# Kernel optimization log

Measured on AMD Instinct MI355X. Metric: run time of the kernel, lower is better.

## Reference

```python
import jax, jax.numpy as jnp
import numpy as np

V, E, H, O, B, T = 50000, 128, 128, 128, 64, 512


def setup_inputs() -> dict:
    key = jax.random.key(0)
    ks = jax.random.split(key, 16)
    s = 0.05
    X = jax.random.randint(ks[0], (B, T), 0, V)
    lens = jnp.sort(jax.random.randint(ks[1], (B,), 64, T + 1))[::-1]
    lens = lens.at[0].set(T)  # pack_padded needs descending lengths, max == T
    emb = jax.random.normal(ks[2], (V, E)) * s
    emb = emb.at[0].set(0.0)  # padding_idx = 0
    return {
        "X": X,
        "X_lengths": lens,
        "batch_size": B,
        "emb": emb,
        "W_e2i": jax.random.normal(ks[3], (H, E)) * s,
        "b_e2i": jax.random.normal(ks[4], (H,)) * s,
        "Wih_f": jax.random.normal(ks[5], (3 * H, H)) * s,
        "Whh_f": jax.random.normal(ks[6], (3 * H, H)) * s,
        "bih_f": jax.random.normal(ks[7], (3 * H,)) * s,
        "bhh_f": jax.random.normal(ks[8], (3 * H,)) * s,
        "Wih_b": jax.random.normal(ks[9], (3 * H, H)) * s,
        "Whh_b": jax.random.normal(ks[10], (3 * H, H)) * s,
        "bih_b": jax.random.normal(ks[11], (3 * H,)) * s,
        "bhh_b": jax.random.normal(ks[12], (3 * H,)) * s,
        "W_h2o": jax.random.normal(ks[13], (O, 2 * H)) * s,
        "b_h2o": jax.random.normal(ks[14], (O,)) * s,
        "u_w": jax.random.uniform(ks[15], (O,)),  # torch.rand
    }


def _gru_scan(gx, mask_tb, Whh, bhh):
    """gx: [T,B,3H] precomputed input gates; mask_tb: [T,B,1] valid-step mask.
    Masked update emulates pack_padded_sequence: padded steps keep h unchanged
    (and h stays 0 before the first valid step of the reversed direction)."""
    h0 = jnp.zeros((gx.shape[1], Whh.shape[1]), gx.dtype)

    def step(h, tb):
        gxt, m = tb
        gh = h @ Whh.T + bhh
        gxr, gxz, gxn = jnp.split(gxt, 3, axis=-1)
        ghr, ghz, ghn = jnp.split(gh, 3, axis=-1)
        r = jax.nn.sigmoid(gxr + ghr)
        z = jax.nn.sigmoid(gxz + ghz)
        n = jnp.tanh(gxn + r * ghn)
        h_new = (1.0 - z) * n + z * h
        h = jnp.where(m, h_new, h)
        return h, h

    _, hs = jax.lax.scan(step, h0, (gx, mask_tb))
    return hs  # [T,B,H]


def reference(X, X_lengths, batch_size, emb, W_e2i, b_e2i,
              Wih_f, Whh_f, bih_f, bhh_f, Wih_b, Whh_b, bih_b, bhh_b,
              W_h2o, b_h2o, u_w):
    x = emb[X]                              # [B,T,E]
    x = x @ W_e2i.T + b_e2i                 # [B,T,H]
    Tn = x.shape[1]
    mask = jnp.arange(Tn)[None, :] < X_lengths[:, None]  # [B,T]
    m_tb = mask.T[:, :, None]               # [T,B,1]

    gx_f = (x @ Wih_f.T + bih_f).transpose(1, 0, 2)       # [T,B,3H]
    h_f = _gru_scan(gx_f, m_tb, Whh_f, bhh_f)             # [T,B,H]
    gx_b = (x @ Wih_b.T + bih_b).transpose(1, 0, 2)[::-1]
    h_b = _gru_scan(gx_b, m_tb[::-1], Whh_b, bhh_b)[::-1]

    Hout = jnp.concatenate([h_f, h_b], axis=-1).transpose(1, 0, 2)  # [B,T,2H]
    Hout = Hout * mask[:, :, None].astype(Hout.dtype)  # pad_packed zeros pads

    Y = jnp.tanh(Hout @ W_h2o.T + b_h2o)               # [B,T,O]
    scores = jnp.where(mask, (Y * u_w).sum(-1), -jnp.inf)  # [B,T]
    alpha = jax.nn.softmax(scores, axis=1)             # per-sample softmax over valid steps
    pooled = jnp.einsum("bt,btd->bd", alpha, Hout)     # [B,2H]
    return pooled[None]                                # [1,B,2H]
```

## Files before the change

### kernel.cpp

```cpp
#include <hip/hip_runtime.h>
#include <hip/hip_bf16.h>

#define VV 50000
#define EE 128
#define HH 128
#define OO 128
#define BB 64
#define TT 512

typedef __bf16 bf16_t;
typedef __attribute__((ext_vector_type(8))) __bf16 bf16x8;
typedef __attribute__((ext_vector_type(4))) __bf16 bf16x4;
typedef __attribute__((ext_vector_type(4))) float floatx4;

#define SC_RZ (-1.4426950408889634f)
#define SC_N  (2.8853900817779268f)

__device__ __forceinline__ bf16x8 ldb8(const bf16_t* p) {
    return *reinterpret_cast<const bf16x8*>(p);
}

__device__ __forceinline__ bf16x8 ldf8_bf(const float* p) {
    const float4* q = reinterpret_cast<const float4*>(p);
    float4 u = q[0], v = q[1];
    bf16x8 r;
    r[0] = (__bf16)u.x; r[1] = (__bf16)u.y; r[2] = (__bf16)u.z; r[3] = (__bf16)u.w;
    r[4] = (__bf16)v.x; r[5] = (__bf16)v.y; r[6] = (__bf16)v.z; r[7] = (__bf16)v.w;
    return r;
}

__device__ __forceinline__ float fast_rcp(float x) { return __builtin_amdgcn_rcpf(x); }
__device__ __forceinline__ float exp2_f(float x) { return __builtin_amdgcn_exp2f(x); }
__device__ __forceinline__ float tanh_f(float x) {
    float e = __expf(2.0f * x);
    return 1.0f - 2.0f * fast_rcp(e + 1.0f);
}

__device__ __forceinline__ void lds_barrier() {
    asm volatile("s_waitcnt lgkmcnt(0)\n\ts_barrier" ::: "memory");
}

__global__ __launch_bounds__(256) void k0_conv(
    const float* __restrict__ we,
    const float* __restrict__ wihf, const float* __restrict__ wihb,
    const float* __restrict__ whhf, const float* __restrict__ whhb,
    const float* __restrict__ wh2o,
    const float* __restrict__ bihf, const float* __restrict__ bhhf,
    const float* __restrict__ bihb, const float* __restrict__ bhhb,
    bf16_t* __restrict__ we_bf,
    bf16_t* __restrict__ wih_bf, bf16_t* __restrict__ whh_bf,
    bf16_t* __restrict__ wh2o_bf, float* __restrict__ gxbias) {
    int tid = blockIdx.x * 256 + threadIdx.x;
    int np = gridDim.x * 256;
    for (int i = tid; i < HH * EE; i += np) we_bf[i] = (bf16_t)we[i];
    for (int i = tid; i < 384 * HH; i += np) {
        int nrow = i >> 7;
        float sc = (nrow < 256) ? SC_RZ : SC_N;
        wih_bf[i] = (bf16_t)(sc * wihf[i]);
        wih_bf[384 * HH + i] = (bf16_t)(sc * wihb[i]);
        whh_bf[i] = (bf16_t)(sc * whhf[i]);
        whh_bf[384 * HH + i] = (bf16_t)(sc * whhb[i]);
    }
    for (int i = tid; i < OO * 256; i += np) wh2o_bf[i] = (bf16_t)wh2o[i];
    if (tid < 768) {
        int dir = tid / 384, n = tid % 384;
        const float* bih = dir ? bihb : bihf;
        const float* bhh = dir ? bhhb : bhhf;
        float sc = (n < 256) ? SC_RZ : SC_N;
        gxbias[tid] = sc * bih[n] + (n < 256 ? sc * bhh[n] : 0.0f);
    }
}

__global__ __launch_bounds__(256) void k12_gx(const int* __restrict__ X,
                                              const float* __restrict__ emb,
                                              const bf16_t* __restrict__ we_bf,
                                              const float* __restrict__ be,
                                              const bf16_t* __restrict__ wih_bf,
                                              const float* __restrict__ gxbias,
                                              const int* __restrict__ lens,
                                              bf16_t* __restrict__ gx3) {
    int blk = blockIdx.x;
    int tq = blk >> 2;
    int g = blk & 3;
    if (4 * tq >= lens[16 * g]) return;

    int lane = threadIdx.x & 63;
    int w2 = threadIdx.x >> 6;
    int quad = lane >> 4, col = lane & 15;

    __shared__ bf16_t xs[4][16 * 136];

#pragma unroll
    for (int tt = 0; tt < 4; ++tt) {
        int t = 4 * tq + tt;
        int v = X[(g * 16 + col) * TT + t];
        bf16x8 a[4];
#pragma unroll
        for (int kc = 0; kc < 4; ++kc)
            a[kc] = ldf8_bf(emb + (size_t)v * EE + kc * 32 + quad * 8);
#pragma unroll
        for (int tl = 0; tl < 2; ++tl) {
            int n = 32 * w2 + 16 * tl + col;
            floatx4 acc = {0.f, 0.f, 0.f, 0.f};
#pragma unroll
            for (int kc = 0; kc < 4; ++kc) {
                bf16x8 bw = ldb8(we_bf + (size_t)n * EE + kc * 32 + quad * 8);
                acc = __builtin_amdgcn_mfma_f32_16x16x32_bf16(a[kc], bw, acc, 0, 0, 0);
            }
            float bias = be[n];
#pragma unroll
            for (int r = 0; r < 4; ++r)
                xs[tt][(quad * 4 + r) * 136 + n] = (bf16_t)(acc[r] + bias);
        }
    }
    __syncthreads();

    bf16x8 a2[4][4];
#pragma unroll
    for (int tt = 0; tt < 4; ++tt)
#pragma unroll
        for (int kc = 0; kc < 4; ++kc)
            a2[tt][kc] = ldb8(xs[tt] + col * 136 + kc * 32 + quad * 8);

#pragma unroll 2
    for (int tl = 0; tl < 12; ++tl) {
        int idx = w2 * 12 + tl;
        int dir = idx >= 24;
        int n = (idx - dir * 24) * 16 + col;
        bf16x8 bw[4];
#pragma unroll
        for (int kc = 0; kc < 4; ++kc)
            bw[kc] = ldb8(wih_bf + ((size_t)dir * 384 + n) * HH + kc * 32 + quad * 8);
        float bias = gxbias[dir * 384 + n];
#pragma unroll
        for (int tt = 0; tt < 4; ++tt) {
            int t = 4 * tq + tt;
            floatx4 acc = {0.f, 0.f, 0.f, 0.f};
#pragma unroll
            for (int kc = 0; kc < 4; ++kc)
                acc = __builtin_amdgcn_mfma_f32_16x16x32_bf16(a2[tt][kc], bw[kc], acc, 0, 0, 0);
            bf16x4 pack;
#pragma unroll
            for (int r = 0; r < 4; ++r)
                pack[r] = (__bf16)(acc[r] + bias);
            *reinterpret_cast<bf16x4*>(
                gx3 + (((size_t)(dir * 16 + 4 * g + quad) * TT + t) * 384 + n) * 4) = pack;
        }
    }
}

#define HPAD 144
#define HBUF (4 * HPAD)
__global__ __launch_bounds__(512) void k3_gru(const bf16_t* __restrict__ gx3,
                                              const bf16_t* __restrict__ whh_bf,
                                              const float* __restrict__ bhh_f,
                                              const float* __restrict__ bhh_b,
                                              const int* __restrict__ lens,
                                              bf16_t* __restrict__ hist2) {
    int g16 = blockIdx.x;
    int dir = blockIdx.y;
    const float* bhh = dir ? bhh_b : bhh_f;

    int tid = threadIdx.x;
    int w = tid >> 6;
    int lane = tid & 63;
    int quad = lane >> 4, col = lane & 15;
    int j = 16 * w + col;

    __shared__ bf16_t hl[2 * HBUF];
    for (int i = tid; i < 2 * HBUF; i += 512) hl[i] = (bf16_t)0.f;

    int len1 = lens[4 * g16 + quad];
    int Lmax = max(max(lens[4 * g16], lens[4 * g16 + 1]),
                   max(lens[4 * g16 + 2], lens[4 * g16 + 3]));

    float bhn = SC_N * bhh[256 + j];

    bf16x8 Bw[3][4];
#pragma unroll
    for (int gate = 0; gate < 3; ++gate)
#pragma unroll
        for (int kc = 0; kc < 4; ++kc)
            Bw[gate][kc] = ldb8(whh_bf + ((size_t)dir * 384 + gate * 128 + j) * HH + kc * 32 + quad * 8);

    const bf16_t* gbase = gx3 + (size_t)(dir * 16 + g16) * TT * 1536;
    bf16_t* hb = hist2 + (size_t)(dir * 16 + g16) * TT * 512;
    int loff[3];
#pragma unroll
    for (int gate = 0; gate < 3; ++gate)
        loff[gate] = (gate * 128 + j) * 4 + quad;
    int hoff = quad * 128 + j;
    int aoff = (col >> 2) * HPAD + quad * 8;

    float h = 0.f;
    int S4 = (Lmax + 3) & ~3;

    __bf16 ring[4][3];
#pragma unroll
    for (int u = 0; u < 4; ++u) {
        int t = dir ? (Lmax - 1 - u) : u;
#pragma unroll
        for (int gate = 0; gate < 3; ++gate)
            ring[u][gate] = gbase[(size_t)t * 1536 + loff[gate]];
    }
    lds_barrier();

    int gstep = dir ? -1536 : 1536;
    int hstep = dir ? -512 : 512;
    const bf16_t* rp0 = gbase + (size_t)(dir ? (Lmax - 5) : 4) * 1536 + loff[0];
    const bf16_t* rp1 = gbase + (size_t)(dir ? (Lmax - 5) : 4) * 1536 + loff[1];
    const bf16_t* rp2 = gbase + (size_t)(dir ? (Lmax - 5) : 4) * 1536 + loff[2];
    bf16_t* hp = hb + (size_t)(dir ? (Lmax - 1) : 0) * 512 + hoff;
    int ulo = dir ? (Lmax - len1) : 0;
    int uhi = dir ? Lmax : len1;

    for (int sb = 0; sb < S4; sb += 4) {
#pragma unroll
        for (int u = 0; u < 4; ++u) {
            int s = sb + u;
            const bf16_t* hc = hl + (s & 1) * HBUF;
            bf16_t* hn = hl + ((s + 1) & 1) * HBUF;

            float gx0 = (float)ring[u][0];
            float gx1 = (float)ring[u][1];
            float gx2 = (float)ring[u][2];

            bf16x8 a[4];
#pragma unroll
            for (int kc = 0; kc < 4; ++kc)
                a[kc] = ldb8(hc + aoff + kc * 32);

            floatx4 cr = {0.f, 0.f, 0.f, 0.f};
            floatx4 cz = {0.f, 0.f, 0.f, 0.f};
            floatx4 cn = {bhn, bhn, bhn, bhn};
#pragma unroll
            for (int kc = 0; kc < 4; ++kc) {
                cr = __builtin_amdgcn_mfma_f32_16x16x32_bf16(a[kc], Bw[0][kc], cr, 0, 0, 0);
                cz = __builtin_amdgcn_mfma_f32_16x16x32_bf16(a[kc], Bw[1][kc], cz, 0, 0, 0);
                cn = __builtin_amdgcn_mfma_f32_16x16x32_bf16(a[kc], Bw[2][kc], cn, 0, 0, 0);
            }

            ring[u][0] = *rp0;
            ring[u][1] = *rp1;
            ring[u][2] = *rp2;
            {
                int adv = (s < Lmax - 5) ? gstep : 0;
                rp0 += adv; rp1 += adv; rp2 += adv;
            }

            float rg = fast_rcp(1.0f + exp2_f(cr[0] + gx0));
            float zg = fast_rcp(1.0f + exp2_f(cz[0] + gx1));
            float v  = fmaf(rg, cn[0], gx2);
            float ng = fmaf(-2.0f, fast_rcp(exp2_f(v) + 1.0f), 1.0f);
            float hnew = fmaf(zg, h - ng, ng);

            bool upd = (s >= ulo) && (s < uhi);
            h = upd ? hnew : h;
            bf16_t h16 = (bf16_t)h;
            hn[quad * HPAD + j] = h16;
            *hp = h16;
            hp += (s < Lmax - 1) ? hstep : 0;

            lds_barrier();
        }
    }
}

__global__ __launch_bounds__(512) void k45_pool(const bf16_t* __restrict__ hist2,
                                                const bf16_t* __restrict__ wh2o_bf,
                                                const float* __restrict__ bh2o,
                                                const float* __restrict__ uw,
                                                const int* __restrict__ lens,
                                                float* __restrict__ out) {
    int b = blockIdx.x;
    int g16 = b >> 2, bl = b & 3;
    int tid = threadIdx.x;
    int lane = tid & 63, w3 = tid >> 6;
    int quad = lane >> 4, col = lane & 15;
    int len = lens[b];

    int p = w3 >> 2;
    int q = w3 & 3;

    __shared__ float smax[TT][4];
    __shared__ float alpha[TT];
    __shared__ float red[512];
    __shared__ float red2[16 * 32 * 8];

    const bf16_t* hf = hist2 + (size_t)g16 * TT * 512 + bl * 128;
    const bf16_t* hbk = hist2 + (size_t)(16 + g16) * TT * 512 + bl * 128;

    int n0 = (q * 2 + 0) * 16 + col;
    int n1 = (q * 2 + 1) * 16 + col;
    float bias0 = bh2o[n0], u0 = uw[n0];
    float bias1 = bh2o[n1], u1 = uw[n1];

    bf16x8 bw0[8], bw1[8];
#pragma unroll
    for (int kc = 0; kc < 8; ++kc) {
        bw0[kc] = ldb8(wh2o_bf + (size_t)n0 * 256 + kc * 32 + quad * 8);
        bw1[kc] = ldb8(wh2o_bf + (size_t)n1 * 256 + kc * 32 + quad * 8);
    }

    int nch = (len + 15) >> 4;
    bf16x8 a[8], an[8];
    {
        int t = p * 16 + col;
#pragma unroll
        for (int kc = 0; kc < 4; ++kc) {
            a[kc]     = ldb8(hf  + (size_t)t * 512 + kc * 32 + quad * 8);
            a[kc + 4] = ldb8(hbk + (size_t)t * 512 + kc * 32 + quad * 8);
        }
    }
    for (int ch = p; ch < nch; ch += 2) {
        int t0 = ch * 16;
        {
            int tn = (ch + 2 < nch ? t0 + 32 : t0) + col;
#pragma unroll
            for (int kc = 0; kc < 4; ++kc) {
                an[kc]     = ldb8(hf  + (size_t)tn * 512 + kc * 32 + quad * 8);
                an[kc + 4] = ldb8(hbk + (size_t)tn * 512 + kc * 32 + quad * 8);
            }
        }
        float p4[4] = {0.f, 0.f, 0.f, 0.f};
#pragma unroll
        for (int tl = 0; tl < 2; ++tl) {
            float bias = tl ? bias1 : bias0;
            float u = tl ? u1 : u0;
            floatx4 acc = {0.f, 0.f, 0.f, 0.f};
#pragma unroll
            for (int kc = 0; kc < 8; ++kc) {
                bf16x8 bw = tl ? bw1[kc] : bw0[kc];
                acc = __builtin_amdgcn_mfma_f32_16x16x32_bf16(a[kc], bw, acc, 0, 0, 0);
            }
#pragma unroll
            for (int r = 0; r < 4; ++r)
                p4[r] += tanh_f(acc[r] + bias) * u;
        }
#pragma unroll
        for (int m = 1; m < 16; m <<= 1)
#pragma unroll
            for (int r = 0; r < 4; ++r)
                p4[r] += __shfl_xor(p4[r], m, 64);
        if (col == 0) {
#pragma unroll
            for (int r = 0; r < 4; ++r)
                smax[t0 + quad * 4 + r][q] = p4[r];
        }
#pragma unroll
        for (int kc = 0; kc < 8; ++kc) a[kc] = an[kc];
    }
    __syncthreads();

    int t = tid;
    float s = -1e30f;
    if (t < len) s = smax[t][0] + smax[t][1] + smax[t][2] + smax[t][3];
    red[tid] = s;
    __syncthreads();
    for (int st = 256; st > 0; st >>= 1) {
        if (tid < st) red[tid] = fmaxf(red[tid], red[tid + st]);
        __syncthreads();
    }
    float mx = red[0];
    __syncthreads();
    float e = (t < len) ? __expf(s - mx) : 0.f;
    alpha[t] = e;
    red[tid] = e;
    __syncthreads();
    for (int st = 256; st > 0; st >>= 1) {
        if (tid < st) red[tid] += red[tid + st];
        __syncthreads();
    }
    float inv = fast_rcp(red[0]);
    __syncthreads();

    {
        int ts = tid >> 5, o = tid & 31;
        int dirp = o >> 4;
        int j8 = (o & 15) * 8;
        const bf16_t* hbase = (dirp ? hbk : hf) + j8;
        float acc8[8];
#pragma unroll
        for (int ee = 0; ee < 8; ++ee) acc8[ee] = 0.f;
        for (int tt2 = ts; tt2 < len; tt2 += 16) {
            float al = alpha[tt2];
            bf16x8 hv = ldb8(hbase + (size_t)tt2 * 512);
#pragma unroll
            for (int ee = 0; ee < 8; ++ee) acc8[ee] = fmaf(al, (float)hv[ee], acc8[ee]);
        }
#pragma unroll
        for (int ee = 0; ee < 8; ++ee) red2[(ts * 32 + o) * 8 + ee] = acc8[ee];
        __syncthreads();
        if (tid < 256) {
            int c = tid;
            int dir2 = c >> 7, rem = c & 127;
            int oo = dir2 * 16 + (rem >> 3), ee = c & 7;
            float acc = 0.f;
#pragma unroll
            for (int qq = 0; qq < 16; ++qq) acc += red2[(qq * 32 + oo) * 8 + ee];
            out[(size_t)b * 256 + c] = acc * inv;
        }
    }
}

extern "C" void kernel_launch(void* const* d_in, const int* in_sizes, int n_in,
                              void* d_out, int out_size, void* d_ws, size_t ws_size,
                              hipStream_t stream) {
    const int* X       = (const int*)d_in[0];
    const int* lens    = (const int*)d_in[1];
    const float* emb   = (const float*)d_in[3];
    const float* We2i  = (const float*)d_in[4];
    const float* be2i  = (const float*)d_in[5];
    const float* Wihf  = (const float*)d_in[6];
    const float* Whhf  = (const float*)d_in[7];
    const float* bihf  = (const float*)d_in[8];
    const float* bhhf  = (const float*)d_in[9];
    const float* Wihb  = (const float*)d_in[10];
    const float* Whhb  = (const float*)d_in[11];
    const float* bihb  = (const float*)d_in[12];
    const float* bhhb  = (const float*)d_in[13];
    const float* Wh2o  = (const float*)d_in[14];
    const float* bh2o  = (const float*)d_in[15];
    const float* uw    = (const float*)d_in[16];

    char* ws = (char*)d_ws;
    size_t off = 0;
    bf16_t* we_bf = (bf16_t*)(ws + off);   off += (size_t)HH * EE * 2;
    bf16_t* wih_bf = (bf16_t*)(ws + off);  off += (size_t)2 * 384 * HH * 2;
    bf16_t* whh_bf = (bf16_t*)(ws + off);  off += (size_t)2 * 384 * HH * 2;
    bf16_t* wh2o_bf = (bf16_t*)(ws + off); off += (size_t)OO * 256 * 2;
    float* gxbias = (float*)(ws + off);    off += 768 * 4;
    off = (off + 255) & ~(size_t)255;
    bf16_t* gx3 = (bf16_t*)(ws + off);     off += (size_t)32 * TT * 384 * 4 * 2;
    bf16_t* hist2 = (bf16_t*)(ws + off);   off += (size_t)32 * TT * 4 * 128 * 2;

    float* out = (float*)d_out;

    k0_conv<<<dim3(256), dim3(256), 0, stream>>>(We2i, Wihf, Wihb, Whhf, Whhb,
                                                 Wh2o, bihf, bhhf, bihb, bhhb,
                                                 we_bf, wih_bf, whh_bf, wh2o_bf, gxbias);
    k12_gx<<<dim3(TT), dim3(256), 0, stream>>>(X, emb, we_bf, be2i, wih_bf, gxbias, lens, gx3);
    k3_gru<<<dim3(16, 2), dim3(512), 0, stream>>>(gx3, whh_bf, bhhf, bhhb, lens, hist2);
    k45_pool<<<dim3(BB), dim3(512), 0, stream>>>(hist2, wh2o_bf, bh2o, uw, lens, out);
}
```

Measured before the change: 342.1 us.

## Drop weight-conversion kernel and convert fp32 weights to bf16 inside consumers

Removes the separate k0_conv launch that pre-converted and pre-scaled all weights to bf16. Each consumer kernel now loads the fp32 weights and applies the scale and bf16 conversion itself, and the gate biases are folded on the fly. k12_gx also goes from 256 to 512 threads, so each wave handles fewer output tiles. This saves one kernel launch plus its global write/read round trip, but it doubles weight-load bytes and adds conversion work inside the other kernels.

```diff
diff --git a/kernel.cpp b/kernel.cpp
--- a/kernel.cpp
+++ b/kernel.cpp
@@ -29,6 +29,17 @@
     return r;
 }
 
+__device__ __forceinline__ bf16x8 ldf8s(const float* p, float s) {
+    const float4* q = reinterpret_cast<const float4*>(p);
+    float4 u = q[0], v = q[1];
+    bf16x8 r;
+    r[0] = (__bf16)(s * u.x); r[1] = (__bf16)(s * u.y);
+    r[2] = (__bf16)(s * u.z); r[3] = (__bf16)(s * u.w);
+    r[4] = (__bf16)(s * v.x); r[5] = (__bf16)(s * v.y);
+    r[6] = (__bf16)(s * v.z); r[7] = (__bf16)(s * v.w);
+    return r;
+}
+
 __device__ __forceinline__ float fast_rcp(float x) { return __builtin_amdgcn_rcpf(x); }
 __device__ __forceinline__ float exp2_f(float x) { return __builtin_amdgcn_exp2f(x); }
 __device__ __forceinline__ float tanh_f(float x) {
@@ -40,43 +51,16 @@
     asm volatile("s_waitcnt lgkmcnt(0)\n\ts_barrier" ::: "memory");
 }
 
-__global__ __launch_bounds__(256) void k0_conv(
-    const float* __restrict__ we,
-    const float* __restrict__ wihf, const float* __restrict__ wihb,
-    const float* __restrict__ whhf, const float* __restrict__ whhb,
-    const float* __restrict__ wh2o,
-    const float* __restrict__ bihf, const float* __restrict__ bhhf,
-    const float* __restrict__ bihb, const float* __restrict__ bhhb,
-    bf16_t* __restrict__ we_bf,
-    bf16_t* __restrict__ wih_bf, bf16_t* __restrict__ whh_bf,
-    bf16_t* __restrict__ wh2o_bf, float* __restrict__ gxbias) {
-    int tid = blockIdx.x * 256 + threadIdx.x;
-    int np = gridDim.x * 256;
-    for (int i = tid; i < HH * EE; i += np) we_bf[i] = (bf16_t)we[i];
-    for (int i = tid; i < 384 * HH; i += np) {
-        int nrow = i >> 7;
-        float sc = (nrow < 256) ? SC_RZ : SC_N;
-        wih_bf[i] = (bf16_t)(sc * wihf[i]);
-        wih_bf[384 * HH + i] = (bf16_t)(sc * wihb[i]);
-        whh_bf[i] = (bf16_t)(sc * whhf[i]);
-        whh_bf[384 * HH + i] = (bf16_t)(sc * whhb[i]);
-    }
-    for (int i = tid; i < OO * 256; i += np) wh2o_bf[i] = (bf16_t)wh2o[i];
-    if (tid < 768) {
-        int dir = tid / 384, n = tid % 384;
-        const float* bih = dir ? bihb : bihf;
-        const float* bhh = dir ? bhhb : bhhf;
-        float sc = (n < 256) ? SC_RZ : SC_N;
-        gxbias[tid] = sc * bih[n] + (n < 256 ? sc * bhh[n] : 0.0f);
-    }
-}
-
-__global__ __launch_bounds__(256) void k12_gx(const int* __restrict__ X,
+__global__ __launch_bounds__(512) void k12_gx(const int* __restrict__ X,
                                               const float* __restrict__ emb,
-                                              const bf16_t* __restrict__ we_bf,
+                                              const float* __restrict__ we,
                                               const float* __restrict__ be,
-                                              const bf16_t* __restrict__ wih_bf,
-                                              const float* __restrict__ gxbias,
+                                              const float* __restrict__ wihf,
+                                              const float* __restrict__ wihb,
+                                              const float* __restrict__ bihf,
+                                              const float* __restrict__ bhhf,
+                                              const float* __restrict__ bihb,
+                                              const float* __restrict__ bhhb,
                                               const int* __restrict__ lens,
                                               bf16_t* __restrict__ gx3) {
     int blk = blockIdx.x;
@@ -84,30 +68,30 @@
     int g = blk & 3;
     if (4 * tq >= lens[16 * g]) return;
 
-    int lane = threadIdx.x & 63;
-    int w2 = threadIdx.x >> 6;
+    int tid = threadIdx.x;
+    int lane = tid & 63;
+    int w = tid >> 6;
     int quad = lane >> 4, col = lane & 15;
 
     __shared__ bf16_t xs[4][16 * 136];
 
-#pragma unroll
-    for (int tt = 0; tt < 4; ++tt) {
-        int t = 4 * tq + tt;
-        int v = X[(g * 16 + col) * TT + t];
-        bf16x8 a[4];
-#pragma unroll
-        for (int kc = 0; kc < 4; ++kc)
-            a[kc] = ldf8_bf(emb + (size_t)v * EE + kc * 32 + quad * 8);
-#pragma unroll
-        for (int tl = 0; tl < 2; ++tl) {
-            int n = 32 * w2 + 16 * tl + col;
+    {
+        int n = 16 * w + col;
+        float bias = be[n];
+#pragma unroll
+        for (int tt = 0; tt < 4; ++tt) {
+            int t = 4 * tq + tt;
+            int v = X[(g * 16 + col) * TT + t];
+            bf16x8 a[4];
+#pragma unroll
+            for (int kc = 0; kc < 4; ++kc)
+                a[kc] = ldf8_bf(emb + (size_t)v * EE + kc * 32 + quad * 8);
             floatx4 acc = {0.f, 0.f, 0.f, 0.f};
 #pragma unroll
             for (int kc = 0; kc < 4; ++kc) {
-                bf16x8 bw = ldb8(we_bf + (size_t)n * EE + kc * 32 + quad * 8);
+                bf16x8 bw = ldf8_bf(we + (size_t)n * EE + kc * 32 + quad * 8);
                 acc = __builtin_amdgcn_mfma_f32_16x16x32_bf16(a[kc], bw, acc, 0, 0, 0);
             }
-            float bias = be[n];
 #pragma unroll
             for (int r = 0; r < 4; ++r)
                 xs[tt][(quad * 4 + r) * 136 + n] = (bf16_t)(acc[r] + bias);
@@ -123,15 +107,19 @@
             a2[tt][kc] = ldb8(xs[tt] + col * 136 + kc * 32 + quad * 8);
 
 #pragma unroll 2
-    for (int tl = 0; tl < 12; ++tl) {
-        int idx = w2 * 12 + tl;
+    for (int tl = 0; tl < 6; ++tl) {
+        int idx = w * 6 + tl;
         int dir = idx >= 24;
         int n = (idx - dir * 24) * 16 + col;
+        const float* wih = dir ? wihb : wihf;
+        const float* bih = dir ? bihb : bihf;
+        const float* bhh = dir ? bhhb : bhhf;
+        float sc = (n < 256) ? SC_RZ : SC_N;
         bf16x8 bw[4];
 #pragma unroll
         for (int kc = 0; kc < 4; ++kc)
-            bw[kc] = ldb8(wih_bf + ((size_t)dir * 384 + n) * HH + kc * 32 + quad * 8);
-        float bias = gxbias[dir * 384 + n];
+            bw[kc] = ldf8s(wih + (size_t)n * HH + kc * 32 + quad * 8, sc);
+        float bias = sc * (bih[n] + (n < 256 ? bhh[n] : 0.0f));
 #pragma unroll
         for (int tt = 0; tt < 4; ++tt) {
             int t = 4 * tq + tt;
@@ -152,7 +140,8 @@
 #define HPAD 144
 #define HBUF (4 * HPAD)
 __global__ __launch_bounds__(512) void k3_gru(const bf16_t* __restrict__ gx3,
-                                              const bf16_t* __restrict__ whh_bf,
+                                              const float* __restrict__ whh_f,
+                                              const float* __restrict__ whh_b,
                                               const float* __restrict__ bhh_f,
                                               const float* __restrict__ bhh_b,
                                               const int* __restrict__ lens,
@@ -160,6 +149,7 @@
     int g16 = blockIdx.x;
     int dir = blockIdx.y;
     const float* bhh = dir ? bhh_b : bhh_f;
+    const float* whh = dir ? whh_b : whh_f;
 
     int tid = threadIdx.x;
     int w = tid >> 6;
@@ -178,10 +168,12 @@
 
     bf16x8 Bw[3][4];
 #pragma unroll
-    for (int gate = 0; gate < 3; ++gate)
+    for (int gate = 0; gate < 3; ++gate) {
+        float sc = (gate < 2) ? SC_RZ : SC_N;
 #pragma unroll
         for (int kc = 0; kc < 4; ++kc)
-            Bw[gate][kc] = ldb8(whh_bf + ((size_t)dir * 384 + gate * 128 + j) * HH + kc * 32 + quad * 8);
+            Bw[gate][kc] = ldf8s(whh + (size_t)(gate * 128 + j) * HH + kc * 32 + quad * 8, sc);
+    }
 
     const bf16_t* gbase = gx3 + (size_t)(dir * 16 + g16) * TT * 1536;
     bf16_t* hb = hist2 + (size_t)(dir * 16 + g16) * TT * 512;
@@ -267,7 +259,7 @@
 }
 
 __global__ __launch_bounds__(512) void k45_pool(const bf16_t* __restrict__ hist2,
-                                                const bf16_t* __restrict__ wh2o_bf,
+                                                const float* __restrict__ wh2o,
                                                 const float* __restrict__ bh2o,
                                                 const float* __restrict__ uw,
                                                 const int* __restrict__ lens,
@@ -298,8 +290,8 @@
     bf16x8 bw0[8], bw1[8];
 #pragma unroll
     for (int kc = 0; kc < 8; ++kc) {
-        bw0[kc] = ldb8(wh2o_bf + (size_t)n0 * 256 + kc * 32 + quad * 8);
-        bw1[kc] = ldb8(wh2o_bf + (size_t)n1 * 256 + kc * 32 + quad * 8);
+        bw0[kc] = ldf8_bf(wh2o + (size_t)n0 * 256 + kc * 32 + quad * 8);
+        bw1[kc] = ldf8_bf(wh2o + (size_t)n1 * 256 + kc * 32 + quad * 8);
     }
 
     int nch = (len + 15) >> 4;
@@ -425,21 +417,13 @@
 
     char* ws = (char*)d_ws;
     size_t off = 0;
-    bf16_t* we_bf = (bf16_t*)(ws + off);   off += (size_t)HH * EE * 2;
-    bf16_t* wih_bf = (bf16_t*)(ws + off);  off += (size_t)2 * 384 * HH * 2;
-    bf16_t* whh_bf = (bf16_t*)(ws + off);  off += (size_t)2 * 384 * HH * 2;
-    bf16_t* wh2o_bf = (bf16_t*)(ws + off); off += (size_t)OO * 256 * 2;
-    float* gxbias = (float*)(ws + off);    off += 768 * 4;
-    off = (off + 255) & ~(size_t)255;
     bf16_t* gx3 = (bf16_t*)(ws + off);     off += (size_t)32 * TT * 384 * 4 * 2;
     bf16_t* hist2 = (bf16_t*)(ws + off);   off += (size_t)32 * TT * 4 * 128 * 2;
 
     float* out = (float*)d_out;
 
-    k0_conv<<<dim3(256), dim3(256), 0, stream>>>(We2i, Wihf, Wihb, Whhf, Whhb,
-                                                 Wh2o, bihf, bhhf, bihb, bhhb,
-                                                 we_bf, wih_bf, whh_bf, wh2o_bf, gxbias);
-    k12_gx<<<dim3(TT), dim3(256), 0, stream>>>(X, emb, we_bf, be2i, wih_bf, gxbias, lens, gx3);
-    k3_gru<<<dim3(16, 2), dim3(512), 0, stream>>>(gx3, whh_bf, bhhf, bhhb, lens, hist2);
-    k45_pool<<<dim3(BB), dim3(512), 0, stream>>>(hist2, wh2o_bf, bh2o, uw, lens, out);
-}
+    k12_gx<<<dim3(TT), dim3(512), 0, stream>>>(X, emb, We2i, be2i, Wihf, Wihb,
+                                               bihf, bhhf, bihb, bhhb, lens, gx3);
+    k3_gru<<<dim3(16, 2), dim3(512), 0, stream>>>(gx3, Whhf, Whhb, bhhf, bhhb, lens, hist2);
+    k45_pool<<<dim3(BB), dim3(512), 0, stream>>>(hist2, Wh2o, bh2o, uw, lens, out);
+}
```

Result: slower. 387.9 us (+13.4%).

## Fuse GRU recurrence and attention pooling into one kernel with atomic grid barrier

Applied to the files above, without the earlier changes.

Merges the GRU scan kernel and the attention-pooling kernel into a single 64-block launch. The first 32 blocks run the recurrence, then every block spin-waits on a global atomic counter, which is reset in the gx kernel, before doing its per-sample pooling. This removes one launch and its gap, but the wait relies on all 64 blocks being co-resident. It also redistributes the embedding projection across waves in k12, splits the h2o MFMA chain into two accumulators, replaces the shared-memory tree reductions with wave shuffles, and pads red2 to avoid bank conflicts.

```diff
diff --git a/kernel.cpp b/kernel.cpp
--- a/kernel.cpp
+++ b/kernel.cpp
@@ -78,7 +78,10 @@
                                               const bf16_t* __restrict__ wih_bf,
                                               const float* __restrict__ gxbias,
                                               const int* __restrict__ lens,
-                                              bf16_t* __restrict__ gx3) {
+                                              bf16_t* __restrict__ gx3,
+                                              unsigned int* __restrict__ ctr) {
+    if (blockIdx.x == 0 && threadIdx.x == 0) *ctr = 0u;
+
     int blk = blockIdx.x;
     int tq = blk >> 2;
     int g = blk & 3;
@@ -90,17 +93,16 @@
 
     __shared__ bf16_t xs[4][16 * 136];
 
-#pragma unroll
-    for (int tt = 0; tt < 4; ++tt) {
-        int t = 4 * tq + tt;
+    {
+        int t = 4 * tq + w2;
         int v = X[(g * 16 + col) * TT + t];
         bf16x8 a[4];
 #pragma unroll
         for (int kc = 0; kc < 4; ++kc)
             a[kc] = ldf8_bf(emb + (size_t)v * EE + kc * 32 + quad * 8);
 #pragma unroll
-        for (int tl = 0; tl < 2; ++tl) {
-            int n = 32 * w2 + 16 * tl + col;
+        for (int nt = 0; nt < 8; ++nt) {
+            int n = nt * 16 + col;
             floatx4 acc = {0.f, 0.f, 0.f, 0.f};
 #pragma unroll
             for (int kc = 0; kc < 4; ++kc) {
@@ -110,7 +112,7 @@
             float bias = be[n];
 #pragma unroll
             for (int r = 0; r < 4; ++r)
-                xs[tt][(quad * 4 + r) * 136 + n] = (bf16_t)(acc[r] + bias);
+                xs[w2][(quad * 4 + r) * 136 + n] = (bf16_t)(acc[r] + bias);
         }
     }
     __syncthreads();
@@ -151,254 +153,265 @@
 
 #define HPAD 144
 #define HBUF (4 * HPAD)
-__global__ __launch_bounds__(512) void k3_gru(const bf16_t* __restrict__ gx3,
-                                              const bf16_t* __restrict__ whh_bf,
-                                              const float* __restrict__ bhh_f,
-                                              const float* __restrict__ bhh_b,
-                                              const int* __restrict__ lens,
-                                              bf16_t* __restrict__ hist2) {
-    int g16 = blockIdx.x;
-    int dir = blockIdx.y;
-    const float* bhh = dir ? bhh_b : bhh_f;
-
+__global__ __launch_bounds__(512) void k345(const bf16_t* __restrict__ gx3,
+                                            const bf16_t* __restrict__ whh_bf,
+                                            const float* __restrict__ bhh_f,
+                                            const float* __restrict__ bhh_b,
+                                            const int* __restrict__ lens,
+                                            const bf16_t* __restrict__ wh2o_bf,
+                                            const float* __restrict__ bh2o,
+                                            const float* __restrict__ uw,
+                                            bf16_t* __restrict__ hist2,
+                                            float* __restrict__ out,
+                                            unsigned int* __restrict__ ctr) {
+    int b = blockIdx.x;
     int tid = threadIdx.x;
-    int w = tid >> 6;
     int lane = tid & 63;
+    int wv = tid >> 6;
     int quad = lane >> 4, col = lane & 15;
-    int j = 16 * w + col;
 
     __shared__ bf16_t hl[2 * HBUF];
-    for (int i = tid; i < 2 * HBUF; i += 512) hl[i] = (bf16_t)0.f;
-
-    int len1 = lens[4 * g16 + quad];
-    int Lmax = max(max(lens[4 * g16], lens[4 * g16 + 1]),
-                   max(lens[4 * g16 + 2], lens[4 * g16 + 3]));
-
-    float bhn = SC_N * bhh[256 + j];
-
-    bf16x8 Bw[3][4];
-#pragma unroll
-    for (int gate = 0; gate < 3; ++gate)
-#pragma unroll
-        for (int kc = 0; kc < 4; ++kc)
-            Bw[gate][kc] = ldb8(whh_bf + ((size_t)dir * 384 + gate * 128 + j) * HH + kc * 32 + quad * 8);
-
-    const bf16_t* gbase = gx3 + (size_t)(dir * 16 + g16) * TT * 1536;
-    bf16_t* hb = hist2 + (size_t)(dir * 16 + g16) * TT * 512;
-    int loff[3];
-#pragma unroll
-    for (int gate = 0; gate < 3; ++gate)
-        loff[gate] = (gate * 128 + j) * 4 + quad;
-    int hoff = quad * 128 + j;
-    int aoff = (col >> 2) * HPAD + quad * 8;
-
-    float h = 0.f;
-    int S4 = (Lmax + 3) & ~3;
-
-    __bf16 ring[4][3];
-#pragma unroll
-    for (int u = 0; u < 4; ++u) {
-        int t = dir ? (Lmax - 1 - u) : u;
-#pragma unroll
-        for (int gate = 0; gate < 3; ++gate)
-            ring[u][gate] = gbase[(size_t)t * 1536 + loff[gate]];
-    }
-    lds_barrier();
-
-    int gstep = dir ? -1536 : 1536;
-    int hstep = dir ? -512 : 512;
-    const bf16_t* rp0 = gbase + (size_t)(dir ? (Lmax - 5) : 4) * 1536 + loff[0];
-    const bf16_t* rp1 = gbase + (size_t)(dir ? (Lmax - 5) : 4) * 1536 + loff[1];
-    const bf16_t* rp2 = gbase + (size_t)(dir ? (Lmax - 5) : 4) * 1536 + loff[2];
-    bf16_t* hp = hb + (size_t)(dir ? (Lmax - 1) : 0) * 512 + hoff;
-    int ulo = dir ? (Lmax - len1) : 0;
-    int uhi = dir ? Lmax : len1;
-
-    for (int sb = 0; sb < S4; sb += 4) {
-#pragma unroll
-        for (int u = 0; u < 4; ++u) {
-            int s = sb + u;
-            const bf16_t* hc = hl + (s & 1) * HBUF;
-            bf16_t* hn = hl + ((s + 1) & 1) * HBUF;
-
-            float gx0 = (float)ring[u][0];
-            float gx1 = (float)ring[u][1];
-            float gx2 = (float)ring[u][2];
-
-            bf16x8 a[4];
-#pragma unroll
-            for (int kc = 0; kc < 4; ++kc)
-                a[kc] = ldb8(hc + aoff + kc * 32);
-
-            floatx4 cr = {0.f, 0.f, 0.f, 0.f};
-            floatx4 cz = {0.f, 0.f, 0.f, 0.f};
-            floatx4 cn = {bhn, bhn, bhn, bhn};
-#pragma unroll
-            for (int kc = 0; kc < 4; ++kc) {
-                cr = __builtin_amdgcn_mfma_f32_16x16x32_bf16(a[kc], Bw[0][kc], cr, 0, 0, 0);
-                cz = __builtin_amdgcn_mfma_f32_16x16x32_bf16(a[kc], Bw[1][kc], cz, 0, 0, 0);
-                cn = __builtin_amdgcn_mfma_f32_16x16x32_bf16(a[kc], Bw[2][kc], cn, 0, 0, 0);
-            }
-
-            ring[u][0] = *rp0;
-            ring[u][1] = *rp1;
-            ring[u][2] = *rp2;
-            {
-                int adv = (s < Lmax - 5) ? gstep : 0;
-                rp0 += adv; rp1 += adv; rp2 += adv;
-            }
-
-            float rg = fast_rcp(1.0f + exp2_f(cr[0] + gx0));
-            float zg = fast_rcp(1.0f + exp2_f(cz[0] + gx1));
-            float v  = fmaf(rg, cn[0], gx2);
-            float ng = fmaf(-2.0f, fast_rcp(exp2_f(v) + 1.0f), 1.0f);
-            float hnew = fmaf(zg, h - ng, ng);
-
-            bool upd = (s >= ulo) && (s < uhi);
-            h = upd ? hnew : h;
-            bf16_t h16 = (bf16_t)h;
-            hn[quad * HPAD + j] = h16;
-            *hp = h16;
-            hp += (s < Lmax - 1) ? hstep : 0;
-
-            lds_barrier();
-        }
-    }
-}
-
-__global__ __launch_bounds__(512) void k45_pool(const bf16_t* __restrict__ hist2,
-                                                const bf16_t* __restrict__ wh2o_bf,
-                                                const float* __restrict__ bh2o,
-                                                const float* __restrict__ uw,
-                                                const int* __restrict__ lens,
-                                                float* __restrict__ out) {
-    int b = blockIdx.x;
-    int g16 = b >> 2, bl = b & 3;
-    int tid = threadIdx.x;
-    int lane = tid & 63, w3 = tid >> 6;
-    int quad = lane >> 4, col = lane & 15;
-    int len = lens[b];
-
-    int p = w3 >> 2;
-    int q = w3 & 3;
-
     __shared__ float smax[TT][4];
     __shared__ float alpha[TT];
-    __shared__ float red[512];
-    __shared__ float red2[16 * 32 * 8];
-
-    const bf16_t* hf = hist2 + (size_t)g16 * TT * 512 + bl * 128;
-    const bf16_t* hbk = hist2 + (size_t)(16 + g16) * TT * 512 + bl * 128;
-
-    int n0 = (q * 2 + 0) * 16 + col;
-    int n1 = (q * 2 + 1) * 16 + col;
-    float bias0 = bh2o[n0], u0 = uw[n0];
-    float bias1 = bh2o[n1], u1 = uw[n1];
-
-    bf16x8 bw0[8], bw1[8];
-#pragma unroll
-    for (int kc = 0; kc < 8; ++kc) {
-        bw0[kc] = ldb8(wh2o_bf + (size_t)n0 * 256 + kc * 32 + quad * 8);
-        bw1[kc] = ldb8(wh2o_bf + (size_t)n1 * 256 + kc * 32 + quad * 8);
-    }
-
-    int nch = (len + 15) >> 4;
-    bf16x8 a[8], an[8];
+    __shared__ float redw[16];
+    __shared__ float red2[16 * 32 * 9];
+
+    if (b < 32) {
+        int g16 = b & 15;
+        int dir = b >> 4;
+        const float* bhh = dir ? bhh_b : bhh_f;
+        int j = 16 * wv + col;
+
+        for (int i = tid; i < 2 * HBUF; i += 512) hl[i] = (bf16_t)0.f;
+
+        int len1 = lens[4 * g16 + quad];
+        int Lmax = max(max(lens[4 * g16], lens[4 * g16 + 1]),
+                       max(lens[4 * g16 + 2], lens[4 * g16 + 3]));
+
+        float bhn = SC_N * bhh[256 + j];
+
+        bf16x8 Bw[3][4];
+#pragma unroll
+        for (int gate = 0; gate < 3; ++gate)
+#pragma unroll
+            for (int kc = 0; kc < 4; ++kc)
+                Bw[gate][kc] = ldb8(whh_bf + ((size_t)dir * 384 + gate * 128 + j) * HH + kc * 32 + quad * 8);
+
+        const bf16_t* gbase = gx3 + (size_t)(dir * 16 + g16) * TT * 1536;
+        bf16_t* hb = hist2 + (size_t)(dir * 16 + g16) * TT * 512;
+        int loff[3];
+#pragma unroll
+        for (int gate = 0; gate < 3; ++gate)
+            loff[gate] = (gate * 128 + j) * 4 + quad;
+        int hoff = quad * 128 + j;
+        int aoff = (col >> 2) * HPAD + quad * 8;
+
+        float h = 0.f;
+        int S4 = (Lmax + 3) & ~3;
+
+        __bf16 ring[4][3];
+#pragma unroll
+        for (int u = 0; u < 4; ++u) {
+            int t = dir ? (Lmax - 1 - u) : u;
+#pragma unroll
+            for (int gate = 0; gate < 3; ++gate)
+                ring[u][gate] = gbase[(size_t)t * 1536 + loff[gate]];
+        }
+        lds_barrier();
+
+        int gstep = dir ? -1536 : 1536;
+        int hstep = dir ? -512 : 512;
+        const bf16_t* rp0 = gbase + (size_t)(dir ? (Lmax - 5) : 4) * 1536 + loff[0];
+        const bf16_t* rp1 = gbase + (size_t)(dir ? (Lmax - 5) : 4) * 1536 + loff[1];
+        const bf16_t* rp2 = gbase + (size_t)(dir ? (Lmax - 5) : 4) * 1536 + loff[2];
+        bf16_t* hp = hb + (size_t)(dir ? (Lmax - 1) : 0) * 512 + hoff;
+        int ulo = dir ? (Lmax - len1) : 0;
+        int uhi = dir ? Lmax : len1;
+
+        for (int sb = 0; sb < S4; sb += 4) {
+#pragma unroll
+            for (int u = 0; u < 4; ++u) {
+                int s = sb + u;
+                const bf16_t* hc = hl + (s & 1) * HBUF;
+                bf16_t* hn = hl + ((s + 1) & 1) * HBUF;
+
+                float gx0 = (float)ring[u][0];
+                float gx1 = (float)ring[u][1];
+                float gx2 = (float)ring[u][2];
+
+                bf16x8 a[4];
+#pragma unroll
+                for (int kc = 0; kc < 4; ++kc)
+                    a[kc] = ldb8(hc + aoff + kc * 32);
+
+                floatx4 cr = {0.f, 0.f, 0.f, 0.f};
+                floatx4 cz = {0.f, 0.f, 0.f, 0.f};
+                floatx4 cn = {bhn, bhn, bhn, bhn};
+#pragma unroll
+                for (int kc = 0; kc < 4; ++kc) {
+                    cr = __builtin_amdgcn_mfma_f32_16x16x32_bf16(a[kc], Bw[0][kc], cr, 0, 0, 0);
+                    cz = __builtin_amdgcn_mfma_f32_16x16x32_bf16(a[kc], Bw[1][kc], cz, 0, 0, 0);
+                    cn = __builtin_amdgcn_mfma_f32_16x16x32_bf16(a[kc], Bw[2][kc], cn, 0, 0, 0);
+                }
+
+                ring[u][0] = *rp0;
+                ring[u][1] = *rp1;
+                ring[u][2] = *rp2;
+                {
+                    int adv = (s < Lmax - 5) ? gstep : 0;
+                    rp0 += adv; rp1 += adv; rp2 += adv;
+                }
+
+                float rg = fast_rcp(1.0f + exp2_f(cr[0] + gx0));
+                float zg = fast_rcp(1.0f + exp2_f(cz[0] + gx1));
+                float v  = fmaf(rg, cn[0], gx2);
+                float ng = fmaf(-2.0f, fast_rcp(exp2_f(v) + 1.0f), 1.0f);
+                float hnew = fmaf(zg, h - ng, ng);
+
+                bool upd = (s >= ulo) && (s < uhi);
+                h = upd ? hnew : h;
+                bf16_t h16 = (bf16_t)h;
+                hn[quad * HPAD + j] = h16;
+                *hp = h16;
+                hp += (s < Lmax - 1) ? hstep : 0;
+
+                lds_barrier();
+            }
+        }
+
+        __threadfence();
+        __syncthreads();
+        if (tid == 0)
+            __hip_atomic_fetch_add(ctr, 1u, __ATOMIC_RELEASE, __HIP_MEMORY_SCOPE_AGENT);
+    }
+
+    if (tid == 0) {
+        while (__hip_atomic_load(ctr, __ATOMIC_ACQUIRE, __HIP_MEMORY_SCOPE_AGENT) < 32u)
+            __builtin_amdgcn_s_sleep(8);
+    }
+    __syncthreads();
+    __threadfence();
+
     {
-        int t = p * 16 + col;
-#pragma unroll
-        for (int kc = 0; kc < 4; ++kc) {
-            a[kc]     = ldb8(hf  + (size_t)t * 512 + kc * 32 + quad * 8);
-            a[kc + 4] = ldb8(hbk + (size_t)t * 512 + kc * 32 + quad * 8);
-        }
-    }
-    for (int ch = p; ch < nch; ch += 2) {
-        int t0 = ch * 16;
+        int g16 = b >> 2, bl = b & 3;
+        int len = lens[b];
+        int p = wv >> 2;
+        int q = wv & 3;
+
+        const bf16_t* hf = hist2 + (size_t)g16 * TT * 512 + bl * 128;
+        const bf16_t* hbk = hist2 + (size_t)(16 + g16) * TT * 512 + bl * 128;
+
+        int n0 = (q * 2 + 0) * 16 + col;
+        int n1 = (q * 2 + 1) * 16 + col;
+        float bias0 = bh2o[n0], u0 = uw[n0];
+        float bias1 = bh2o[n1], u1 = uw[n1];
+
+        bf16x8 bw0[8], bw1[8];
+#pragma unroll
+        for (int kc = 0; kc < 8; ++kc) {
+            bw0[kc] = ldb8(wh2o_bf + (size_t)n0 * 256 + kc * 32 + quad * 8);
+            bw1[kc] = ldb8(wh2o_bf + (size_t)n1 * 256 + kc * 32 + quad * 8);
+        }
+
+        int nch = (len + 15) >> 4;
+        bf16x8 a[8], an[8];
         {
-            int tn = (ch + 2 < nch ? t0 + 32 : t0) + col;
+            int t = p * 16 + col;
 #pragma unroll
             for (int kc = 0; kc < 4; ++kc) {
-                an[kc]     = ldb8(hf  + (size_t)tn * 512 + kc * 32 + quad * 8);
-                an[kc + 4] = ldb8(hbk + (size_t)tn * 512 + kc * 32 + quad * 8);
-            }
-        }
-        float p4[4] = {0.f, 0.f, 0.f, 0.f};
-#pragma unroll
-        for (int tl = 0; tl < 2; ++tl) {
-            float bias = tl ? bias1 : bias0;
-            float u = tl ? u1 : u0;
-            floatx4 acc = {0.f, 0.f, 0.f, 0.f};
-#pragma unroll
-            for (int kc = 0; kc < 8; ++kc) {
-                bf16x8 bw = tl ? bw1[kc] : bw0[kc];
-                acc = __builtin_amdgcn_mfma_f32_16x16x32_bf16(a[kc], bw, acc, 0, 0, 0);
-            }
-#pragma unroll
-            for (int r = 0; r < 4; ++r)
-                p4[r] += tanh_f(acc[r] + bias) * u;
-        }
-#pragma unroll
-        for (int m = 1; m < 16; m <<= 1)
-#pragma unroll
-            for (int r = 0; r < 4; ++r)
-                p4[r] += __shfl_xor(p4[r], m, 64);
-        if (col == 0) {
-#pragma unroll
-            for (int r = 0; r < 4; ++r)
-                smax[t0 + quad * 4 + r][q] = p4[r];
-        }
-#pragma unroll
-        for (int kc = 0; kc < 8; ++kc) a[kc] = an[kc];
-    }
-    __syncthreads();
-
-    int t = tid;
-    float s = -1e30f;
-    if (t < len) s = smax[t][0] + smax[t][1] + smax[t][2] + smax[t][3];
-    red[tid] = s;
-    __syncthreads();
-    for (int st = 256; st > 0; st >>= 1) {
-        if (tid < st) red[tid] = fmaxf(red[tid], red[tid + st]);
+                a[kc]     = ldb8(hf  + (size_t)t * 512 + kc * 32 + quad * 8);
+                a[kc + 4] = ldb8(hbk + (size_t)t * 512 + kc * 32 + quad * 8);
+            }
+        }
+        for (int ch = p; ch < nch; ch += 2) {
+            int t0 = ch * 16;
+            {
+                int tn = (ch + 2 < nch ? t0 + 32 : t0) + col;
+#pragma unroll
+                for (int kc = 0; kc < 4; ++kc) {
+                    an[kc]     = ldb8(hf  + (size_t)tn * 512 + kc * 32 + quad * 8);
+                    an[kc + 4] = ldb8(hbk + (size_t)tn * 512 + kc * 32 + quad * 8);
+                }
+            }
+            float p4[4] = {0.f, 0.f, 0.f, 0.f};
+#pragma unroll
+            for (int tl = 0; tl < 2; ++tl) {
+                float bias = tl ? bias1 : bias0;
+                float u = tl ? u1 : u0;
+                floatx4 accA = {0.f, 0.f, 0.f, 0.f};
+                floatx4 accB = {0.f, 0.f, 0.f, 0.f};
+#pragma unroll
+                for (int kc = 0; kc < 4; ++kc) {
+                    bf16x8 bwA = tl ? bw1[kc] : bw0[kc];
+                    bf16x8 bwB = tl ? bw1[kc + 4] : bw0[kc + 4];
+                    accA = __builtin_amdgcn_mfma_f32_16x16x32_bf16(a[kc], bwA, accA, 0, 0, 0);
+                    accB = __builtin_amdgcn_mfma_f32_16x16x32_bf16(a[kc + 4], bwB, accB, 0, 0, 0);
+                }
+#pragma unroll
+                for (int r = 0; r < 4; ++r)
+                    p4[r] += tanh_f(accA[r] + accB[r] + bias) * u;
+            }
+#pragma unroll
+            for (int m = 1; m < 16; m <<= 1)
+#pragma unroll
+                for (int r = 0; r < 4; ++r)
+                    p4[r] += __shfl_xor(p4[r], m, 64);
+            if (col == 0) {
+#pragma unroll
+                for (int r = 0; r < 4; ++r)
+                    smax[t0 + quad * 4 + r][q] = p4[r];
+            }
+#pragma unroll
+            for (int kc = 0; kc < 8; ++kc) a[kc] = an[kc];
+        }
         __syncthreads();
-    }
-    float mx = red[0];
-    __syncthreads();
-    float e = (t < len) ? __expf(s - mx) : 0.f;
-    alpha[t] = e;
-    red[tid] = e;
-    __syncthreads();
-    for (int st = 256; st > 0; st >>= 1) {
-        if (tid < st) red[tid] += red[tid + st];
+
+        int t = tid;
+        float s = -1e30f;
+        if (t < len) s = smax[t][0] + smax[t][1] + smax[t][2] + smax[t][3];
+        float m = s;
+#pragma unroll
+        for (int off = 1; off <= 32; off <<= 1) m = fmaxf(m, __shfl_xor(m, off, 64));
+        if (lane == 0) redw[wv] = m;
         __syncthreads();
-    }
-    float inv = fast_rcp(red[0]);
-    __syncthreads();
-
-    {
-        int ts = tid >> 5, o = tid & 31;
-        int dirp = o >> 4;
-        int j8 = (o & 15) * 8;
-        const bf16_t* hbase = (dirp ? hbk : hf) + j8;
-        float acc8[8];
-#pragma unroll
-        for (int ee = 0; ee < 8; ++ee) acc8[ee] = 0.f;
-        for (int tt2 = ts; tt2 < len; tt2 += 16) {
-            float al = alpha[tt2];
-            bf16x8 hv = ldb8(hbase + (size_t)tt2 * 512);
-#pragma unroll
-            for (int ee = 0; ee < 8; ++ee) acc8[ee] = fmaf(al, (float)hv[ee], acc8[ee]);
-        }
-#pragma unroll
-        for (int ee = 0; ee < 8; ++ee) red2[(ts * 32 + o) * 8 + ee] = acc8[ee];
+        float mx = fmaxf(fmaxf(fmaxf(redw[0], redw[1]), fmaxf(redw[2], redw[3])),
+                         fmaxf(fmaxf(redw[4], redw[5]), fmaxf(redw[6], redw[7])));
+        float e = (t < len) ? __expf(s - mx) : 0.f;
+        alpha[t] = e;
+        float sm = e;
+#pragma unroll
+        for (int off = 1; off <= 32; off <<= 1) sm += __shfl_xor(sm, off, 64);
+        if (lane == 0) redw[8 + wv] = sm;
         __syncthreads();
-        if (tid < 256) {
-            int c = tid;
-            int dir2 = c >> 7, rem = c & 127;
-            int oo = dir2 * 16 + (rem >> 3), ee = c & 7;
-            float acc = 0.f;
-#pragma unroll
-            for (int qq = 0; qq < 16; ++qq) acc += red2[(qq * 32 + oo) * 8 + ee];
-            out[(size_t)b * 256 + c] = acc * inv;
+        float inv = fast_rcp(redw[8] + redw[9] + redw[10] + redw[11] +
+                             redw[12] + redw[13] + redw[14] + redw[15]);
+
+        {
+            int ts = tid >> 5, o = tid & 31;
+            int dirp = o >> 4;
+            int j8 = (o & 15) * 8;
+            const bf16_t* hbase = (dirp ? hbk : hf) + j8;
+            float acc8[8];
+#pragma unroll
+            for (int ee = 0; ee < 8; ++ee) acc8[ee] = 0.f;
+            for (int tt2 = ts; tt2 < len; tt2 += 16) {
+                float al = alpha[tt2];
+                bf16x8 hv = ldb8(hbase + (size_t)tt2 * 512);
+#pragma unroll
+                for (int ee = 0; ee < 8; ++ee) acc8[ee] = fmaf(al, (float)hv[ee], acc8[ee]);
+            }
+#pragma unroll
+            for (int ee = 0; ee < 8; ++ee) red2[(ts * 32 + o) * 9 + ee] = acc8[ee];
+            __syncthreads();
+            if (tid < 256) {
+                int c = tid;
+                int dir2 = c >> 7, rem = c & 127;
+                int oo = dir2 * 16 + (rem >> 3), ee = c & 7;
+                float acc = 0.f;
+#pragma unroll
+                for (int qq = 0; qq < 16; ++qq) acc += red2[(qq * 32 + oo) * 9 + ee];
+                out[(size_t)b * 256 + c] = acc * inv;
+            }
         }
     }
 }
@@ -431,6 +444,7 @@
     bf16_t* wh2o_bf = (bf16_t*)(ws + off); off += (size_t)OO * 256 * 2;
     float* gxbias = (float*)(ws + off);    off += 768 * 4;
     off = (off + 255) & ~(size_t)255;
+    unsigned int* ctr = (unsigned int*)(ws + off); off += 256;
     bf16_t* gx3 = (bf16_t*)(ws + off);     off += (size_t)32 * TT * 384 * 4 * 2;
     bf16_t* hist2 = (bf16_t*)(ws + off);   off += (size_t)32 * TT * 4 * 128 * 2;
 
@@ -439,7 +453,7 @@
     k0_conv<<<dim3(256), dim3(256), 0, stream>>>(We2i, Wihf, Wihb, Whhf, Whhb,
                                                  Wh2o, bihf, bhhf, bihb, bhhb,
                                                  we_bf, wih_bf, whh_bf, wh2o_bf, gxbias);
-    k12_gx<<<dim3(TT), dim3(256), 0, stream>>>(X, emb, we_bf, be2i, wih_bf, gxbias, lens, gx3);
-    k3_gru<<<dim3(16, 2), dim3(512), 0, stream>>>(gx3, whh_bf, bhhf, bhhb, lens, hist2);
-    k45_pool<<<dim3(BB), dim3(512), 0, stream>>>(hist2, wh2o_bf, bh2o, uw, lens, out);
-}
+    k12_gx<<<dim3(TT), dim3(256), 0, stream>>>(X, emb, we_bf, be2i, wih_bf, gxbias, lens, gx3, ctr);
+    k345<<<dim3(BB), dim3(512), 0, stream>>>(gx3, whh_bf, bhhf, bhhb, lens,
+                                             wh2o_bf, bh2o, uw, hist2, out, ctr);
+}
```

Result: slower. 373.0 us (+9.0%).
